# Kernel tuning notes

Measured on AMD Instinct MI355X. Metric: run time of the kernel, lower is better.

The kernel has to match this reference:

```python
import jax, jax.numpy as jnp
import numpy as np

N_HARMONIC = 6
CONCAT = (3,)  # cfg.append_distance: concat embedding after this layer index
N_LAYERS = 8


def harmonic_embedding(x):
    # x: [N, 3] -> [N, 6*2*3 + 3] = [N, 39]
    freqs = 2.0 ** jnp.arange(N_HARMONIC, dtype=x.dtype)  # omega0 = 1.0, logspace
    embed = (x[..., None] * freqs).reshape(*x.shape[:-1], -1)  # [N, 18]
    return jnp.concatenate([jnp.sin(embed), jnp.cos(embed), x], axis=-1)


def setup_inputs() -> dict:
    key = jax.random.key(0)
    N, H, E = 262144, 256, 39
    ks = jax.random.split(key, 11)
    inp = {"points": jax.random.normal(ks[0], (N, 3), dtype=jnp.float32)}
    in_dims = [E, H, H, H, E + H, H, H, H]  # skip-concat before layer 4
    for i, d_in in enumerate(in_dims):
        scale = 1.0 / np.sqrt(d_in)
        inp[f"w{i}"] = jax.random.normal(ks[i + 1], (d_in, H), dtype=jnp.float32) * scale
        inp[f"b{i}"] = jnp.zeros((H,), dtype=jnp.float32)
    inp["wsdf"] = jax.random.normal(ks[9], (H, 1), dtype=jnp.float32) * (1.0 / np.sqrt(H))
    inp["bsdf"] = jnp.zeros((1,), dtype=jnp.float32)
    return inp


def reference(points, w0, b0, w1, b1, w2, b2, w3, b3, w4, b4, w5, b5, w6, b6, w7, b7, wsdf, bsdf):
    ws = [w0, w1, w2, w3, w4, w5, w6, w7]
    bs = [b0, b1, b2, b3, b4, b5, b6, b7]
    emb = harmonic_embedding(points.reshape(-1, 3))  # [N, 39]
    x = emb
    for i in range(N_LAYERS):
        x = jax.nn.relu(x @ ws[i] + bs[i])
        if i in CONCAT:
            x = jnp.concatenate([emb, x], axis=-1)  # torch.cat([add, xyz])
    return x @ wsdf + bsdf  # [N, 1] signed distance
```

## Files before the change

kernel.cpp:

```cpp
#include <hip/hip_runtime.h>
#include <hip/hip_fp16.h>

typedef _Float16 f16x8 __attribute__((ext_vector_type(8)));
typedef _Float16 f16x4 __attribute__((ext_vector_type(4)));
typedef _Float16 f16x2 __attribute__((ext_vector_type(2)));
typedef float    f32x16 __attribute__((ext_vector_type(16)));
typedef float    f32x4 __attribute__((ext_vector_type(4)));

#define SH 264
#define SE 56

struct LayerPtrs {
  const float* w[8];
  const float* b[8];
};

__global__ void prep_weights(LayerPtrs P, f16x8* __restrict__ wf) {
  int gid = blockIdx.x * 256 + threadIdx.x;
  if (gid >= 60416) return;
  const int OFF[9] = {0,1536,9728,17920,26112,35840,44032,52224,60416};
  int l = 0;
  while (gid >= OFF[l+1]) ++l;
  int f = gid - OFF[l];
  int lane = f & 63;
  int t = f >> 6;
  int mtile = t & 7;
  int kc = t >> 3;
  int col = mtile * 32 + (lane & 31);
  int kb  = (lane >> 5) * 8;
  const float* w = P.w[l];
  f16x8 v;
#pragma unroll
  for (int j = 0; j < 8; ++j) {
    float x = 0.f;
    if (l == 4) {
      if (kc < 3) {
        int k = kc * 16 + kb + j;
        if (k < 39) x = w[k * 256 + col];
      } else {
        int k = (kc - 3) * 16 + kb + j;
        x = w[(39 + k) * 256 + col];
      }
    } else if (l == 0) {
      int k = kc * 16 + kb + j;
      if (k < 39) x = w[k * 256 + col];
    } else {
      int k = kc * 16 + kb + j;
      x = w[k * 256 + col];
    }
    v[j] = (_Float16)x;
  }
  wf[gid] = v;
}

#define MFMA __builtin_amdgcn_mfma_f32_32x32x16_f16

__device__ __forceinline__ void aload2(f16x8& d0, f16x8& d1, const f16x8* p) {
  asm volatile("global_load_dwordx4 %0, %2, off\n\t"
               "global_load_dwordx4 %1, %2, off offset:1024"
               : "=&v"(d0), "=&v"(d1)
               : "v"(p));
}

struct APre { f16x8 a00, a01, a10, a11; };

__device__ __forceinline__ APre apre(const f16x8* __restrict__ wb) {
  APre p;
  aload2(p.a00, p.a01, wb);
  aload2(p.a10, p.a11, wb + 512);
  return p;
}

__device__ __forceinline__ void mfma8(f16x8 a0, f16x8 a1,
                                      f16x8 v0, f16x8 v1, f16x8 v2, f16x8 v3,
                                      f32x16 acc[2][4]) {
  __builtin_amdgcn_s_setprio(1);
  acc[0][0] = MFMA(a0, v0, acc[0][0], 0, 0, 0);
  acc[0][1] = MFMA(a0, v1, acc[0][1], 0, 0, 0);
  acc[0][2] = MFMA(a0, v2, acc[0][2], 0, 0, 0);
  acc[0][3] = MFMA(a0, v3, acc[0][3], 0, 0, 0);
  acc[1][0] = MFMA(a1, v0, acc[1][0], 0, 0, 0);
  acc[1][1] = MFMA(a1, v1, acc[1][1], 0, 0, 0);
  acc[1][2] = MFMA(a1, v2, acc[1][2], 0, 0, 0);
  acc[1][3] = MFMA(a1, v3, acc[1][3], 0, 0, 0);
  __builtin_amdgcn_s_setprio(0);
}

__device__ __forceinline__ void mfma8_z(f16x8 a0, f16x8 a1,
                                        f16x8 v0, f16x8 v1, f16x8 v2, f16x8 v3,
                                        f32x16 acc[2][4]) {
  const f32x16 z = {};
  __builtin_amdgcn_s_setprio(1);
  acc[0][0] = MFMA(a0, v0, z, 0, 0, 0);
  acc[0][1] = MFMA(a0, v1, z, 0, 0, 0);
  acc[0][2] = MFMA(a0, v2, z, 0, 0, 0);
  acc[0][3] = MFMA(a0, v3, z, 0, 0, 0);
  acc[1][0] = MFMA(a1, v0, z, 0, 0, 0);
  acc[1][1] = MFMA(a1, v1, z, 0, 0, 0);
  acc[1][2] = MFMA(a1, v2, z, 0, 0, 0);
  acc[1][3] = MFMA(a1, v3, z, 0, 0, 0);
  __builtin_amdgcn_s_setprio(0);
}

template<int NKC, bool FIRST, int RSTRIDE>
__device__ __forceinline__ void mm(const f16x8* __restrict__ wb,
                                   const char* __restrict__ r0,
                                   f32x16 acc[2][4], APre p) {
  f16x8 a00 = p.a00, a01 = p.a01, a10 = p.a10, a11 = p.a11;
  f16x8 v0 = *(const f16x8*)(r0);
  f16x8 v1 = *(const f16x8*)(r0 + RSTRIDE);
  f16x8 v2 = *(const f16x8*)(r0 + 2 * RSTRIDE);
  f16x8 v3 = *(const f16x8*)(r0 + 3 * RSTRIDE);
#pragma unroll
  for (int kc = 0; kc < NKC; ++kc) {
    f16x8 na0, na1, nv0, nv1, nv2, nv3;
    if (kc + 2 < NKC) aload2(na0, na1, wb + (kc + 2) * 512);
    if (kc + 1 < NKC) {
      const char* rp = r0 + 32 * (kc + 1);
      nv0 = *(const f16x8*)(rp);
      nv1 = *(const f16x8*)(rp + RSTRIDE);
      nv2 = *(const f16x8*)(rp + 2 * RSTRIDE);
      nv3 = *(const f16x8*)(rp + 3 * RSTRIDE);
    }
    if (kc + 2 < NKC)      asm volatile("s_waitcnt vmcnt(4)");
    else if (kc + 1 < NKC) asm volatile("s_waitcnt vmcnt(2)");
    else                   asm volatile("s_waitcnt vmcnt(0)");
    __builtin_amdgcn_sched_barrier(0);
    if (FIRST && kc == 0) mfma8_z(a00, a01, v0, v1, v2, v3, acc);
    else                  mfma8 (a00, a01, v0, v1, v2, v3, acc);
    if (kc + 1 < NKC) {
      a00 = a10; a01 = a11;
      v0 = nv0; v1 = nv1; v2 = nv2; v3 = nv3;
    }
    if (kc + 2 < NKC) { a10 = na0; a11 = na1; }
  }
}

template<int RSE, int RSH>
__device__ __forceinline__ void mm4(const f16x8* __restrict__ wb,
                                    const char* __restrict__ eR,
                                    const char* __restrict__ hR,
                                    f32x16 acc[2][4], APre p) {
  constexpr int NKC = 19;
  f16x8 a00 = p.a00, a01 = p.a01, a10 = p.a10, a11 = p.a11;
  f16x8 v0 = *(const f16x8*)(eR);
  f16x8 v1 = *(const f16x8*)(eR + RSE);
  f16x8 v2 = *(const f16x8*)(eR + 2 * RSE);
  f16x8 v3 = *(const f16x8*)(eR + 3 * RSE);
#pragma unroll
  for (int kc = 0; kc < NKC; ++kc) {
    f16x8 na0, na1, nv0, nv1, nv2, nv3;
    if (kc + 2 < NKC) aload2(na0, na1, wb + (kc + 2) * 512);
    if (kc + 1 < NKC) {
      if (kc + 1 < 3) {
        const char* rp = eR + 32 * (kc + 1);
        nv0 = *(const f16x8*)(rp);
        nv1 = *(const f16x8*)(rp + RSE);
        nv2 = *(const f16x8*)(rp + 2 * RSE);
        nv3 = *(const f16x8*)(rp + 3 * RSE);
      } else {
        const char* rp = hR + 32 * (kc + 1 - 3);
        nv0 = *(const f16x8*)(rp);
        nv1 = *(const f16x8*)(rp + RSH);
        nv2 = *(const f16x8*)(rp + 2 * RSH);
        nv3 = *(const f16x8*)(rp + 3 * RSH);
      }
    }
    if (kc + 2 < NKC)      asm volatile("s_waitcnt vmcnt(4)");
    else if (kc + 1 < NKC) asm volatile("s_waitcnt vmcnt(2)");
    else                   asm volatile("s_waitcnt vmcnt(0)");
    __builtin_amdgcn_sched_barrier(0);
    if (kc == 0) mfma8_z(a00, a01, v0, v1, v2, v3, acc);
    else         mfma8 (a00, a01, v0, v1, v2, v3, acc);
    if (kc + 1 < NKC) {
      a00 = a10; a01 = a11;
      v0 = nv0; v1 = nv1; v2 = nv2; v3 = nv3;
    }
    if (kc + 2 < NKC) { a10 = na0; a11 = na1; }
  }
}

__device__ __forceinline__ f16x4 relu_cvt4(f32x4 s) {
  f16x2 lo = __builtin_bit_cast(f16x2, __builtin_amdgcn_cvt_pkrtz(s[0], s[1]));
  f16x2 hi = __builtin_bit_cast(f16x2, __builtin_amdgcn_cvt_pkrtz(s[2], s[3]));
  union { f16x4 v; f16x2 h[2]; } u;
  u.h[0] = lo; u.h[1] = hi;
  f16x4 z = {};
  return __builtin_elementwise_max(u.v, z);
}

__device__ __forceinline__ void store_epi(f32x16 acc[2][4],
                                          const float* __restrict__ bias,
                                          int wg, int p0, int h,
                                          _Float16* __restrict__ Hs) {
#pragma unroll
  for (int mt = 0; mt < 2; ++mt) {
    int hb = wg * 64 + mt * 32 + 4 * h;
#pragma unroll
    for (int g = 0; g < 4; ++g) {
      f32x4 q = *(const f32x4*)&bias[hb + 8 * g];
#pragma unroll
      for (int nt = 0; nt < 4; ++nt) {
        f32x4 s = {acc[mt][nt][4 * g + 0], acc[mt][nt][4 * g + 1],
                   acc[mt][nt][4 * g + 2], acc[mt][nt][4 * g + 3]};
        *(f16x4*)&Hs[(nt * 32 + p0) * SH + hb + 8 * g] = relu_cvt4(s + q);
      }
    }
  }
}

__device__ __forceinline__ void emb_channel(_Float16* __restrict__ Erow,
                                            int c, float x) {
  _Float16 sv[6], cv[6];
  float fr = 1.f;
#pragma unroll
  for (int k = 0; k < 6; ++k) {
    float e = x * fr;
    sv[k] = (_Float16)__sinf(e);
    cv[k] = (_Float16)__cosf(e);
    fr *= 2.f;
  }
#pragma unroll
  for (int k = 0; k < 6; k += 2) {
    f16x2 s2 = {sv[k], sv[k + 1]};
    f16x2 c2 = {cv[k], cv[k + 1]};
    *(f16x2*)&Erow[6 * c + k]      = s2;
    *(f16x2*)&Erow[18 + 6 * c + k] = c2;
  }
  Erow[36 + c] = (_Float16)x;
}

__global__ __launch_bounds__(256, 2)
void mlp_fused(const float* __restrict__ points,
               LayerPtrs P,
               const f16x8* __restrict__ wf,
               const float* __restrict__ wsdf,
               const float* __restrict__ bsdf,
               float* __restrict__ out) {
  __shared__ __align__(16) _Float16 Hs[128 * SH];
  __shared__ __align__(16) _Float16 Es[128 * SE];
  const int tid = threadIdx.x;
  const int blk = blockIdx.x;

  const int lane = tid & 63;
  const int wg   = tid >> 6;
  const int p0   = lane & 31;
  const int h    = lane >> 5;

  const f16x8* wb = wf + wg * 128 + lane;
  const int WOFF[8] = {0, 1536, 9728, 17920, 26112, 35840, 44032, 52224};

  APre ap = apre(wb);

  {
    int p = tid & 127, part = tid >> 7;
    _Float16* Erow = &Es[p * SE];
    const float* pp = &points[(blk * 128 + p) * 3];
    if (part == 0) {
      emb_channel(Erow, 0, pp[0]);
      emb_channel(Erow, 1, pp[1]);
    } else {
      emb_channel(Erow, 2, pp[2]);
      Erow[39] = (_Float16)0.f;
      f16x4 z4 = {};
      *(f16x4*)&Erow[40] = z4;
      *(f16x4*)&Erow[44] = z4;
      *(f16x4*)&Erow[48] = z4;
      *(f16x4*)&Erow[52] = z4;
    }
  }
  __syncthreads();

  const char* hR = (const char*)Hs + (p0 * SH + 8 * h) * 2;
  const char* eR = (const char*)Es + (p0 * SE + 8 * h) * 2;

  f32x16 acc[2][4];

  mm<3, true, 32 * SE * 2>(wb, eR, acc, ap);
  ap = apre(wb + WOFF[1]);
  store_epi(acc, P.b[0], wg, p0, h, Hs);
  __syncthreads();

#pragma unroll
  for (int l = 1; l < 4; ++l) {
    mm<16, true, 32 * SH * 2>(wb + WOFF[l], hR, acc, ap);
    ap = apre(wb + WOFF[l + 1]);
    __syncthreads();
    store_epi(acc, P.b[l], wg, p0, h, Hs);
    __syncthreads();
  }

  {
    mm4<32 * SE * 2, 32 * SH * 2>(wb + 26112, eR, hR, acc, ap);
    ap = apre(wb + WOFF[5]);
    __syncthreads();
    store_epi(acc, P.b[4], wg, p0, h, Hs);
    __syncthreads();
  }

#pragma unroll
  for (int l = 5; l < 7; ++l) {
    mm<16, true, 32 * SH * 2>(wb + WOFF[l], hR, acc, ap);
    ap = apre(wb + WOFF[l + 1]);
    __syncthreads();
    store_epi(acc, P.b[l], wg, p0, h, Hs);
    __syncthreads();
  }

  mm<16, true, 32 * SH * 2>(wb + 52224, hR, acc, ap);
  {
    float part[4] = {0.f, 0.f, 0.f, 0.f};
    const float* b7 = P.b[7];
#pragma unroll
    for (int mt = 0; mt < 2; ++mt) {
#pragma unroll
      for (int g = 0; g < 4; ++g) {
        int idx = wg * 64 + mt * 32 + 8 * g + 4 * h;
        f32x4 qb = *(const f32x4*)&b7[idx];
        f32x4 qw = *(const f32x4*)&wsdf[idx];
#pragma unroll
        for (int nt = 0; nt < 4; ++nt)
#pragma unroll
          for (int r = 0; r < 4; ++r)
            part[nt] += fmaxf(acc[mt][nt][4 * g + r] + qb[r], 0.f) * qw[r];
      }
    }
    float* PB = (float*)Es;
#pragma unroll
    for (int nt = 0; nt < 4; ++nt)
      PB[(wg * 2 + h) * 128 + nt * 32 + p0] = part[nt];
    __syncthreads();
    if (tid < 128) {
      float s = bsdf[0];
#pragma unroll
      for (int j = 0; j < 8; ++j) s += PB[j * 128 + tid];
      out[blk * 128 + tid] = s;
    }
  }
}

extern "C" void kernel_launch(void* const* d_in, const int* in_sizes, int n_in,
                              void* d_out, int out_size, void* d_ws, size_t ws_size,
                              hipStream_t stream) {
  const float* points = (const float*)d_in[0];
  LayerPtrs P;
  for (int i = 0; i < 8; ++i) {
    P.w[i] = (const float*)d_in[1 + 2 * i];
    P.b[i] = (const float*)d_in[2 + 2 * i];
  }
  const float* wsdf = (const float*)d_in[17];
  const float* bsdf = (const float*)d_in[18];
  f16x8* wf = (f16x8*)d_ws;

  int N = in_sizes[0] / 3;
  prep_weights<<<236, 256, 0, stream>>>(P, wf);
  mlp_fused<<<N / 128, 256, 0, stream>>>(points, P, wf, wsdf, bsdf, (float*)d_out);
}
```

Baseline: 298.0 us.

## Fold bias into MFMA accumulator init and replace syncthreads with lgkm barriers

Bias vectors for each layer are prefetched with inline-asm global loads alongside the weight prefetch and used as the initial MFMA accumulator, removing the per-element bias add and the bias loads from the epilogue. Full __syncthreads are replaced by an LDS-only wait plus s_barrier, so outstanding global weight and bias prefetches no longer have to drain at each barrier. The s_setprio hints around the MFMA groups are also removed. The bias registers raise register pressure, and the hand-written vmcnt counts in the matmul loops now also cover the extra bias loads in flight, which the code relies on to stay correct.

```diff
diff --git a/kernel.cpp b/kernel.cpp
--- a/kernel.cpp
+++ b/kernel.cpp
@@ -63,7 +63,6 @@
 }
 
 struct APre { f16x8 a00, a01, a10, a11; };
-
 __device__ __forceinline__ APre apre(const f16x8* __restrict__ wb) {
   APre p;
   aload2(p.a00, p.a01, wb);
@@ -71,10 +70,33 @@
   return p;
 }
 
+struct BQ { f32x4 q[2][4]; };
+__device__ __forceinline__ BQ bload(const float* __restrict__ bp) {
+  BQ b;
+  asm volatile("global_load_dwordx4 %0, %8, off\n\t"
+               "global_load_dwordx4 %1, %8, off offset:32\n\t"
+               "global_load_dwordx4 %2, %8, off offset:64\n\t"
+               "global_load_dwordx4 %3, %8, off offset:96\n\t"
+               "global_load_dwordx4 %4, %8, off offset:128\n\t"
+               "global_load_dwordx4 %5, %8, off offset:160\n\t"
+               "global_load_dwordx4 %6, %8, off offset:192\n\t"
+               "global_load_dwordx4 %7, %8, off offset:224"
+               : "=&v"(b.q[0][0]), "=&v"(b.q[0][1]),
+                 "=&v"(b.q[0][2]), "=&v"(b.q[0][3]),
+                 "=&v"(b.q[1][0]), "=&v"(b.q[1][1]),
+                 "=&v"(b.q[1][2]), "=&v"(b.q[1][3])
+               : "v"(bp));
+  return b;
+}
+
+__device__ __forceinline__ void barrier_lgkm() {
+  asm volatile("s_waitcnt lgkmcnt(0)" ::: "memory");
+  __builtin_amdgcn_s_barrier();
+}
+
 __device__ __forceinline__ void mfma8(f16x8 a0, f16x8 a1,
                                       f16x8 v0, f16x8 v1, f16x8 v2, f16x8 v3,
                                       f32x16 acc[2][4]) {
-  __builtin_amdgcn_s_setprio(1);
   acc[0][0] = MFMA(a0, v0, acc[0][0], 0, 0, 0);
   acc[0][1] = MFMA(a0, v1, acc[0][1], 0, 0, 0);
   acc[0][2] = MFMA(a0, v2, acc[0][2], 0, 0, 0);
@@ -83,29 +105,33 @@
   acc[1][1] = MFMA(a1, v1, acc[1][1], 0, 0, 0);
   acc[1][2] = MFMA(a1, v2, acc[1][2], 0, 0, 0);
   acc[1][3] = MFMA(a1, v3, acc[1][3], 0, 0, 0);
-  __builtin_amdgcn_s_setprio(0);
-}
-
-__device__ __forceinline__ void mfma8_z(f16x8 a0, f16x8 a1,
+}
+
+__device__ __forceinline__ void mfma8_c(f16x8 a0, f16x8 a1,
                                         f16x8 v0, f16x8 v1, f16x8 v2, f16x8 v3,
-                                        f32x16 acc[2][4]) {
-  const f32x16 z = {};
-  __builtin_amdgcn_s_setprio(1);
-  acc[0][0] = MFMA(a0, v0, z, 0, 0, 0);
-  acc[0][1] = MFMA(a0, v1, z, 0, 0, 0);
-  acc[0][2] = MFMA(a0, v2, z, 0, 0, 0);
-  acc[0][3] = MFMA(a0, v3, z, 0, 0, 0);
-  acc[1][0] = MFMA(a1, v0, z, 0, 0, 0);
-  acc[1][1] = MFMA(a1, v1, z, 0, 0, 0);
-  acc[1][2] = MFMA(a1, v2, z, 0, 0, 0);
-  acc[1][3] = MFMA(a1, v3, z, 0, 0, 0);
-  __builtin_amdgcn_s_setprio(0);
-}
-
-template<int NKC, bool FIRST, int RSTRIDE>
+                                        f32x16 acc[2][4], const BQ& bq) {
+  f32x16 c0, c1;
+#pragma unroll
+  for (int g = 0; g < 4; ++g)
+#pragma unroll
+    for (int r = 0; r < 4; ++r) {
+      c0[4 * g + r] = bq.q[0][g][r];
+      c1[4 * g + r] = bq.q[1][g][r];
+    }
+  acc[0][0] = MFMA(a0, v0, c0, 0, 0, 0);
+  acc[0][1] = MFMA(a0, v1, c0, 0, 0, 0);
+  acc[0][2] = MFMA(a0, v2, c0, 0, 0, 0);
+  acc[0][3] = MFMA(a0, v3, c0, 0, 0, 0);
+  acc[1][0] = MFMA(a1, v0, c1, 0, 0, 0);
+  acc[1][1] = MFMA(a1, v1, c1, 0, 0, 0);
+  acc[1][2] = MFMA(a1, v2, c1, 0, 0, 0);
+  acc[1][3] = MFMA(a1, v3, c1, 0, 0, 0);
+}
+
+template<int NKC, int RSTRIDE>
 __device__ __forceinline__ void mm(const f16x8* __restrict__ wb,
                                    const char* __restrict__ r0,
-                                   f32x16 acc[2][4], APre p) {
+                                   f32x16 acc[2][4], const BQ& bq, APre p) {
   f16x8 a00 = p.a00, a01 = p.a01, a10 = p.a10, a11 = p.a11;
   f16x8 v0 = *(const f16x8*)(r0);
   f16x8 v1 = *(const f16x8*)(r0 + RSTRIDE);
@@ -126,8 +152,8 @@
     else if (kc + 1 < NKC) asm volatile("s_waitcnt vmcnt(2)");
     else                   asm volatile("s_waitcnt vmcnt(0)");
     __builtin_amdgcn_sched_barrier(0);
-    if (FIRST && kc == 0) mfma8_z(a00, a01, v0, v1, v2, v3, acc);
-    else                  mfma8 (a00, a01, v0, v1, v2, v3, acc);
+    if (kc == 0) mfma8_c(a00, a01, v0, v1, v2, v3, acc, bq);
+    else         mfma8 (a00, a01, v0, v1, v2, v3, acc);
     if (kc + 1 < NKC) {
       a00 = a10; a01 = a11;
       v0 = nv0; v1 = nv1; v2 = nv2; v3 = nv3;
@@ -140,7 +166,7 @@
 __device__ __forceinline__ void mm4(const f16x8* __restrict__ wb,
                                     const char* __restrict__ eR,
                                     const char* __restrict__ hR,
-                                    f32x16 acc[2][4], APre p) {
+                                    f32x16 acc[2][4], const BQ& bq, APre p) {
   constexpr int NKC = 19;
   f16x8 a00 = p.a00, a01 = p.a01, a10 = p.a10, a11 = p.a11;
   f16x8 v0 = *(const f16x8*)(eR);
@@ -170,7 +196,7 @@
     else if (kc + 1 < NKC) asm volatile("s_waitcnt vmcnt(2)");
     else                   asm volatile("s_waitcnt vmcnt(0)");
     __builtin_amdgcn_sched_barrier(0);
-    if (kc == 0) mfma8_z(a00, a01, v0, v1, v2, v3, acc);
+    if (kc == 0) mfma8_c(a00, a01, v0, v1, v2, v3, acc, bq);
     else         mfma8 (a00, a01, v0, v1, v2, v3, acc);
     if (kc + 1 < NKC) {
       a00 = a10; a01 = a11;
@@ -180,9 +206,9 @@
   }
 }
 
-__device__ __forceinline__ f16x4 relu_cvt4(f32x4 s) {
-  f16x2 lo = __builtin_bit_cast(f16x2, __builtin_amdgcn_cvt_pkrtz(s[0], s[1]));
-  f16x2 hi = __builtin_bit_cast(f16x2, __builtin_amdgcn_cvt_pkrtz(s[2], s[3]));
+__device__ __forceinline__ f16x4 relu_cvt4(float a0, float a1, float a2, float a3) {
+  f16x2 lo = __builtin_bit_cast(f16x2, __builtin_amdgcn_cvt_pkrtz(a0, a1));
+  f16x2 hi = __builtin_bit_cast(f16x2, __builtin_amdgcn_cvt_pkrtz(a2, a3));
   union { f16x4 v; f16x2 h[2]; } u;
   u.h[0] = lo; u.h[1] = hi;
   f16x4 z = {};
@@ -190,7 +216,6 @@
 }
 
 __device__ __forceinline__ void store_epi(f32x16 acc[2][4],
-                                          const float* __restrict__ bias,
                                           int wg, int p0, int h,
                                           _Float16* __restrict__ Hs) {
 #pragma unroll
@@ -198,12 +223,11 @@
     int hb = wg * 64 + mt * 32 + 4 * h;
 #pragma unroll
     for (int g = 0; g < 4; ++g) {
-      f32x4 q = *(const f32x4*)&bias[hb + 8 * g];
 #pragma unroll
       for (int nt = 0; nt < 4; ++nt) {
-        f32x4 s = {acc[mt][nt][4 * g + 0], acc[mt][nt][4 * g + 1],
-                   acc[mt][nt][4 * g + 2], acc[mt][nt][4 * g + 3]};
-        *(f16x4*)&Hs[(nt * 32 + p0) * SH + hb + 8 * g] = relu_cvt4(s + q);
+        f16x4 o = relu_cvt4(acc[mt][nt][4 * g + 0], acc[mt][nt][4 * g + 1],
+                            acc[mt][nt][4 * g + 2], acc[mt][nt][4 * g + 3]);
+        *(f16x4*)&Hs[(nt * 32 + p0) * SH + hb + 8 * g] = o;
       }
     }
   }
@@ -249,8 +273,7 @@
 
   const f16x8* wb = wf + wg * 128 + lane;
   const int WOFF[8] = {0, 1536, 9728, 17920, 26112, 35840, 44032, 52224};
-
-  APre ap = apre(wb);
+  const float* bbase = nullptr;
 
   {
     int p = tid & 127, part = tid >> 7;
@@ -269,67 +292,71 @@
       *(f16x4*)&Erow[52] = z4;
     }
   }
-  __syncthreads();
+
+  BQ   bq = bload(P.b[0] + wg * 64 + 4 * h);
+  APre ap = apre(wb);
+  barrier_lgkm();
 
   const char* hR = (const char*)Hs + (p0 * SH + 8 * h) * 2;
   const char* eR = (const char*)Es + (p0 * SE + 8 * h) * 2;
 
   f32x16 acc[2][4];
 
-  mm<3, true, 32 * SE * 2>(wb, eR, acc, ap);
+  mm<3, 32 * SE * 2>(wb, eR, acc, bq, ap);
+  bq = bload(P.b[1] + wg * 64 + 4 * h);
   ap = apre(wb + WOFF[1]);
-  store_epi(acc, P.b[0], wg, p0, h, Hs);
-  __syncthreads();
+  store_epi(acc, wg, p0, h, Hs);
+  barrier_lgkm();
 
 #pragma unroll
   for (int l = 1; l < 4; ++l) {
-    mm<16, true, 32 * SH * 2>(wb + WOFF[l], hR, acc, ap);
+    mm<16, 32 * SH * 2>(wb + WOFF[l], hR, acc, bq, ap);
+    bq = bload(P.b[l + 1] + wg * 64 + 4 * h);
     ap = apre(wb + WOFF[l + 1]);
-    __syncthreads();
-    store_epi(acc, P.b[l], wg, p0, h, Hs);
-    __syncthreads();
+    barrier_lgkm();
+    store_epi(acc, wg, p0, h, Hs);
+    barrier_lgkm();
   }
 
   {
-    mm4<32 * SE * 2, 32 * SH * 2>(wb + 26112, eR, hR, acc, ap);
+    mm4<32 * SE * 2, 32 * SH * 2>(wb + 26112, eR, hR, acc, bq, ap);
+    bq = bload(P.b[5] + wg * 64 + 4 * h);
     ap = apre(wb + WOFF[5]);
-    __syncthreads();
-    store_epi(acc, P.b[4], wg, p0, h, Hs);
-    __syncthreads();
+    barrier_lgkm();
+    store_epi(acc, wg, p0, h, Hs);
+    barrier_lgkm();
   }
 
 #pragma unroll
   for (int l = 5; l < 7; ++l) {
-    mm<16, true, 32 * SH * 2>(wb + WOFF[l], hR, acc, ap);
+    mm<16, 32 * SH * 2>(wb + WOFF[l], hR, acc, bq, ap);
+    bq = bload(P.b[l + 1] + wg * 64 + 4 * h);
     ap = apre(wb + WOFF[l + 1]);
-    __syncthreads();
-    store_epi(acc, P.b[l], wg, p0, h, Hs);
-    __syncthreads();
-  }
-
-  mm<16, true, 32 * SH * 2>(wb + 52224, hR, acc, ap);
+    barrier_lgkm();
+    store_epi(acc, wg, p0, h, Hs);
+    barrier_lgkm();
+  }
+
+  mm<16, 32 * SH * 2>(wb + 52224, hR, acc, bq, ap);
   {
     float part[4] = {0.f, 0.f, 0.f, 0.f};
-    const float* b7 = P.b[7];
 #pragma unroll
     for (int mt = 0; mt < 2; ++mt) {
 #pragma unroll
       for (int g = 0; g < 4; ++g) {
-        int idx = wg * 64 + mt * 32 + 8 * g + 4 * h;
-        f32x4 qb = *(const f32x4*)&b7[idx];
-        f32x4 qw = *(const f32x4*)&wsdf[idx];
+        f32x4 qw = *(const f32x4*)&wsdf[wg * 64 + mt * 32 + 8 * g + 4 * h];
 #pragma unroll
         for (int nt = 0; nt < 4; ++nt)
 #pragma unroll
           for (int r = 0; r < 4; ++r)
-            part[nt] += fmaxf(acc[mt][nt][4 * g + r] + qb[r], 0.f) * qw[r];
+            part[nt] += fmaxf(acc[mt][nt][4 * g + r], 0.f) * qw[r];
       }
     }
     float* PB = (float*)Es;
 #pragma unroll
     for (int nt = 0; nt < 4; ++nt)
       PB[(wg * 2 + h) * 128 + nt * 32 + p0] = part[nt];
-    __syncthreads();
+    barrier_lgkm();
     if (tid < 128) {
       float s = bsdf[0];
 #pragma unroll
```

New measurement: 295.2 us. No clear change (-0.9%).
